# Kernel optimization log

Measured on AMD Instinct MI355X. Metric: run time of the kernel, lower is better.

Reference implementation:

```python
import jax, jax.numpy as jnp
import numpy as np

B, S, K, N, GROUP = 4, 8, 4096, 11008, 128
NUM_GROUPS = K // GROUP  # 32


def setup_inputs() -> dict:
    key = jax.random.key(0)
    k1, k2, k3 = jax.random.split(key, 3)
    x = jax.random.normal(k1, (B, S, K), dtype=jnp.float16)
    # packed int4 weights: each byte holds two nibbles (low nibble = even k, high = odd k)
    weight_packed = jax.random.randint(k2, (N, K // 2), 0, 256, dtype=jnp.int32)
    # scales: abs(randn)*0.1 in fp16, as in the torch module
    scales = (jnp.abs(jax.random.normal(k3, (N, NUM_GROUPS), dtype=jnp.float16)) * jnp.float16(0.1))
    return {"x": x, "weight_packed": weight_packed, "scales": scales}


def _dequant(weight_packed, scales, Kd):
    # unpack: low nibble -> even index k, high nibble -> odd index k+1
    n = weight_packed.shape[0]
    low = weight_packed & 0xF
    high = (weight_packed >> 4) & 0xF
    w = jnp.stack([low, high], axis=-1).reshape(n, Kd)  # [N, K] int in [0,16)
    g = Kd // scales.shape[1]
    # group-wise dequant: scale * (w - 8), scale applied in fp32 (matches fp32-accum kernel)
    wq = (w.astype(jnp.float32) - 8.0).reshape(n, scales.shape[1], g)
    wdeq = wq * scales.astype(jnp.float32)[:, :, None]
    return wdeq.reshape(n, Kd)  # [N, K] fp32


def reference(x, weight_packed, scales):
    b, s, kd = x.shape
    wdeq = _dequant(weight_packed, scales, kd)           # [N, K]
    x2 = x.reshape(-1, kd).astype(jnp.float32)           # [M, K], fp32 accumulation
    out = jnp.einsum('mk,nk->mn', x2, wdeq)              # [M, N]
    return out.astype(jnp.float16).reshape(b, s, -1)
```

## Files before the change

### kernel.cpp

```cpp
#include <hip/hip_runtime.h>

#define M 32
#define N 11008
#define K 4096
#define NGROUPS 32
#define BN 16
#define KW 1024

typedef _Float16 half8 __attribute__((ext_vector_type(8)));
typedef float floatx4 __attribute__((ext_vector_type(4)));

__global__ __launch_bounds__(256) void int4_gemm_kernel(
    const float* __restrict__ x,
    const int* __restrict__ wp,
    const float* __restrict__ scales,
    float* __restrict__ out)
{
    __shared__ float red[4 * M * BN];

    const int t    = threadIdx.x;
    const int lane = t & 63;
    const int w    = t >> 6;
    const int n0   = blockIdx.x * BN;
    const int row  = lane & 15;
    const int quad = lane >> 4;

    const int* wrow     = wp + (long)(n0 + row) * (K / 2) + (w * (KW / 2)) + quad * 4;
    const float* srow   = scales + (n0 + row) * NGROUPS + w * (KW / 128);
    const float* xr0    = x + row * K + w * KW + quad * 8;
    const float* xr1    = xr0 + 16 * K;

    floatx4 acc0 = {0.f, 0.f, 0.f, 0.f};
    floatx4 acc1 = {0.f, 0.f, 0.f, 0.f};

    #pragma unroll 2
    for (int g = 0; g < KW / 128; ++g) {
        const float s = srow[g];
        floatx4 t0 = {0.f, 0.f, 0.f, 0.f};
        floatx4 t1 = {0.f, 0.f, 0.f, 0.f};
        #pragma unroll
        for (int kk = 0; kk < 4; ++kk) {
            const int koff = g * 128 + kk * 32;
            int4 b4 = *(const int4*)(wrow + (koff >> 1));
            int arr[4] = {b4.x, b4.y, b4.z, b4.w};
            half8 bfrag;
            #pragma unroll
            for (int j = 0; j < 4; ++j) {
                bfrag[2 * j]     = (_Float16)((arr[j] & 15) - 8);
                bfrag[2 * j + 1] = (_Float16)(((arr[j] >> 4) & 15) - 8);
            }
            float4 u0 = *(const float4*)(xr0 + koff);
            float4 u1 = *(const float4*)(xr0 + koff + 4);
            float4 v0 = *(const float4*)(xr1 + koff);
            float4 v1 = *(const float4*)(xr1 + koff + 4);
            half8 a0, a1;
            a0[0] = (_Float16)u0.x; a0[1] = (_Float16)u0.y;
            a0[2] = (_Float16)u0.z; a0[3] = (_Float16)u0.w;
            a0[4] = (_Float16)u1.x; a0[5] = (_Float16)u1.y;
            a0[6] = (_Float16)u1.z; a0[7] = (_Float16)u1.w;
            a1[0] = (_Float16)v0.x; a1[1] = (_Float16)v0.y;
            a1[2] = (_Float16)v0.z; a1[3] = (_Float16)v0.w;
            a1[4] = (_Float16)v1.x; a1[5] = (_Float16)v1.y;
            a1[6] = (_Float16)v1.z; a1[7] = (_Float16)v1.w;

            t0 = __builtin_amdgcn_mfma_f32_16x16x32_f16(a0, bfrag, t0, 0, 0, 0);
            t1 = __builtin_amdgcn_mfma_f32_16x16x32_f16(a1, bfrag, t1, 0, 0, 0);
        }
        #pragma unroll
        for (int r = 0; r < 4; ++r) {
            acc0[r] += s * t0[r];
            acc1[r] += s * t1[r];
        }
    }

    #pragma unroll
    for (int r = 0; r < 4; ++r) {
        red[w * (M * BN) + (quad * 4 + r) * BN + row]      = acc0[r];
        red[w * (M * BN) + (quad * 4 + r + 16) * BN + row] = acc1[r];
    }
    __syncthreads();

    #pragma unroll
    for (int i = 0; i < 2; ++i) {
        int o = t + 256 * i;
        float sum = red[o] + red[M * BN + o] + red[2 * M * BN + o] + red[3 * M * BN + o];
        int m = o >> 4;
        int n = o & 15;
        out[m * N + n0 + n] = sum;
    }
}

extern "C" void kernel_launch(void* const* d_in, const int* in_sizes, int n_in,
                              void* d_out, int out_size, void* d_ws, size_t ws_size,
                              hipStream_t stream) {
    const float* x      = (const float*)d_in[0];
    const int* wp       = (const int*)d_in[1];
    const float* scales = (const float*)d_in[2];
    float* out          = (float*)d_out;

    int4_gemm_kernel<<<dim3(N / BN), 256, 0, stream>>>(x, wp, scales, out);
}
```

Before: 169.1 us.

## Pre-convert activations to fp16 in workspace and split K across 8 waves

Adds a small pre-pass kernel that converts x from fp32 to fp16 once into the workspace. The GEMM then loads half8 fragments directly instead of re-reading and converting fp32 x in every block. The GEMM block also grows to 8 waves, each covering 512 of K, with an 8-way shared-memory reduction. This halves the activation bytes each block reads and adds parallelism per block, at the cost of an extra kernel launch and a larger reduction.

```diff
diff --git a/kernel.cpp b/kernel.cpp
--- a/kernel.cpp
+++ b/kernel.cpp
@@ -5,18 +5,31 @@
 #define K 4096
 #define NGROUPS 32
 #define BN 16
-#define KW 1024
+#define WAVES 8
+#define KW 512
 
 typedef _Float16 half8 __attribute__((ext_vector_type(8)));
+typedef _Float16 half4 __attribute__((ext_vector_type(4)));
 typedef float floatx4 __attribute__((ext_vector_type(4)));
 
-__global__ __launch_bounds__(256) void int4_gemm_kernel(
-    const float* __restrict__ x,
+__global__ __launch_bounds__(512) void xcvt_kernel(
+    const float* __restrict__ x, _Float16* __restrict__ xf)
+{
+    int i = (blockIdx.x * 512 + threadIdx.x) * 4;
+    float4 v = *(const float4*)(x + i);
+    half4 h;
+    h[0] = (_Float16)v.x; h[1] = (_Float16)v.y;
+    h[2] = (_Float16)v.z; h[3] = (_Float16)v.w;
+    *(half4*)(xf + i) = h;
+}
+
+__global__ __launch_bounds__(512, 6) void int4_gemm_kernel(
+    const _Float16* __restrict__ x,
     const int* __restrict__ wp,
     const float* __restrict__ scales,
     float* __restrict__ out)
 {
-    __shared__ float red[4 * M * BN];
+    __shared__ float red[WAVES * M * BN];
 
     const int t    = threadIdx.x;
     const int lane = t & 63;
@@ -25,15 +38,15 @@
     const int row  = lane & 15;
     const int quad = lane >> 4;
 
-    const int* wrow     = wp + (long)(n0 + row) * (K / 2) + (w * (KW / 2)) + quad * 4;
-    const float* srow   = scales + (n0 + row) * NGROUPS + w * (KW / 128);
-    const float* xr0    = x + row * K + w * KW + quad * 8;
-    const float* xr1    = xr0 + 16 * K;
+    const int* wrow        = wp + (long)(n0 + row) * (K / 2) + w * (KW / 2) + quad * 4;
+    const float* srow      = scales + (n0 + row) * NGROUPS + w * (KW / 128);
+    const _Float16* xr0    = x + row * K + w * KW + quad * 8;
+    const _Float16* xr1    = xr0 + 16 * K;
 
     floatx4 acc0 = {0.f, 0.f, 0.f, 0.f};
     floatx4 acc1 = {0.f, 0.f, 0.f, 0.f};
 
-    #pragma unroll 2
+    #pragma unroll
     for (int g = 0; g < KW / 128; ++g) {
         const float s = srow[g];
         floatx4 t0 = {0.f, 0.f, 0.f, 0.f};
@@ -49,20 +62,8 @@
                 bfrag[2 * j]     = (_Float16)((arr[j] & 15) - 8);
                 bfrag[2 * j + 1] = (_Float16)(((arr[j] >> 4) & 15) - 8);
             }
-            float4 u0 = *(const float4*)(xr0 + koff);
-            float4 u1 = *(const float4*)(xr0 + koff + 4);
-            float4 v0 = *(const float4*)(xr1 + koff);
-            float4 v1 = *(const float4*)(xr1 + koff + 4);
-            half8 a0, a1;
-            a0[0] = (_Float16)u0.x; a0[1] = (_Float16)u0.y;
-            a0[2] = (_Float16)u0.z; a0[3] = (_Float16)u0.w;
-            a0[4] = (_Float16)u1.x; a0[5] = (_Float16)u1.y;
-            a0[6] = (_Float16)u1.z; a0[7] = (_Float16)u1.w;
-            a1[0] = (_Float16)v0.x; a1[1] = (_Float16)v0.y;
-            a1[2] = (_Float16)v0.z; a1[3] = (_Float16)v0.w;
-            a1[4] = (_Float16)v1.x; a1[5] = (_Float16)v1.y;
-            a1[6] = (_Float16)v1.z; a1[7] = (_Float16)v1.w;
-
+            half8 a0 = *(const half8*)(xr0 + koff);
+            half8 a1 = *(const half8*)(xr1 + koff);
             t0 = __builtin_amdgcn_mfma_f32_16x16x32_f16(a0, bfrag, t0, 0, 0, 0);
             t1 = __builtin_amdgcn_mfma_f32_16x16x32_f16(a1, bfrag, t1, 0, 0, 0);
         }
@@ -80,12 +81,12 @@
     }
     __syncthreads();
 
-    #pragma unroll
-    for (int i = 0; i < 2; ++i) {
-        int o = t + 256 * i;
-        float sum = red[o] + red[M * BN + o] + red[2 * M * BN + o] + red[3 * M * BN + o];
-        int m = o >> 4;
-        int n = o & 15;
+    {
+        float sum = 0.f;
+        #pragma unroll
+        for (int i = 0; i < WAVES; ++i) sum += red[i * (M * BN) + t];
+        int m = t >> 4;
+        int n = t & 15;
         out[m * N + n0 + n] = sum;
     }
 }
@@ -97,6 +98,8 @@
     const int* wp       = (const int*)d_in[1];
     const float* scales = (const float*)d_in[2];
     float* out          = (float*)d_out;
+    _Float16* xf16      = (_Float16*)d_ws;
 
-    int4_gemm_kernel<<<dim3(N / BN), 256, 0, stream>>>(x, wp, scales, out);
+    xcvt_kernel<<<dim3((M * K) / (512 * 4)), 512, 0, stream>>>(x, xf16);
+    int4_gemm_kernel<<<dim3(N / BN), 512, 0, stream>>>(xf16, wp, scales, out);
 }
```

New measurement: 158.8 us. 1.06x faster.
